# Optimization experiments

Hardware: AMD Instinct MI355X
Metric: run time of the kernel (lower is better)

The kernel has to match this reference:

```python
import jax, jax.numpy as jnp
import numpy as np

N_NODES = 50000
N_EDGES = 800000
N_GRAPHS = 256
D_IN, D_H1, D_H2, D_OUT = 64, 64, 64, 64


def gcn_conv(x, W, b, src, dst, n_nodes):
    # PyG GCNConv (eval): h = x @ W; add self-loops; deg[i] = in_deg(i) + 1;
    # out[i] = sum_{j->i} h[j] * deg[i]^-1/2 deg[j]^-1/2 + h[i]/deg[i] + b
    h = x @ W  # [N, F]
    ones = jnp.ones((src.shape[0],), dtype=x.dtype)
    deg = jax.ops.segment_sum(ones, dst, num_segments=n_nodes) + 1.0  # self loop
    dinv = jax.lax.rsqrt(deg)
    norm = dinv[src] * dinv[dst]  # [E]
    msg = h[src] * norm[:, None]  # [E, F]  (memory-bound gather)
    agg = jax.ops.segment_sum(msg, dst, num_segments=n_nodes)  # scatter-add
    agg = agg + h * (1.0 / deg)[:, None]  # self-loop contribution
    return agg + b


def setup_inputs() -> dict:
    key = jax.random.key(0)
    ks = jax.random.split(key, 12)
    x = jax.random.normal(ks[0], (N_NODES, D_IN), dtype=jnp.float32)
    src = jax.random.randint(ks[1], (N_EDGES,), 0, N_NODES)
    dst = jax.random.randint(ks[2], (N_EDGES,), 0, N_NODES)
    batch = jnp.sort(jax.random.randint(ks[3], (N_NODES,), 0, N_GRAPHS))
    def glorot(k, fin, fout):
        s = jnp.sqrt(6.0 / (fin + fout))
        return jax.random.uniform(k, (fin, fout), jnp.float32, -s, s)
    return {
        "x": x, "src": src, "dst": dst, "batch": batch,
        "W1": glorot(ks[4], D_IN, D_H1), "b1": jnp.zeros((D_H1,), jnp.float32),
        "W2": glorot(ks[5], D_H1, D_H2), "b2": jnp.zeros((D_H2,), jnp.float32),
        "W3": glorot(ks[6], D_H2, D_OUT), "b3": jnp.zeros((D_OUT,), jnp.float32),
        "Wl": glorot(ks[7], D_OUT, 1), "bl": jnp.zeros((1,), jnp.float32),
    }


def reference(x, src, dst, batch, W1, b1, W2, b2, W3, b3, Wl, bl):
    n = x.shape[0]
    h = jax.nn.relu(gcn_conv(x, W1, b1, src, dst, n))   # dropout inactive (eval)
    h = jax.nn.relu(gcn_conv(h, W2, b2, src, dst, n))
    h = jax.nn.relu(gcn_conv(h, W3, b3, src, dst, n))
    # global_mean_pool over graph ids
    sums = jax.ops.segment_sum(h, batch, num_segments=N_GRAPHS)  # [G, F]
    cnt = jax.ops.segment_sum(jnp.ones((n,), h.dtype), batch, num_segments=N_GRAPHS)
    pooled = sums / jnp.maximum(cnt, 1.0)[:, None]
    return pooled @ Wl + bl  # [G, 1]
```

## Files before the change

kernel.cpp:

```cpp
#include <hip/hip_runtime.h>

#define N_NODES 50000
#define N_EDGES 800000
#define N_GRAPHS 256
#define F 64
#define NBUCK 196
#define CAP 5120
#define P3_TILE 2048
#define P3_GRID ((N_EDGES + P3_TILE - 1) / P3_TILE)
#define BCAP 6144
#define ZOFF (N_NODES * 128)

__device__ __forceinline__ unsigned short f2bf(float f) {
    union { float f; unsigned u; } c; c.f = f;
    unsigned u = c.u + 0x7FFFu + ((c.u >> 16) & 1u);
    return (unsigned short)(u >> 16);
}
__device__ __forceinline__ unsigned pack2bf(float lo, float hi) {
    return (unsigned)f2bf(lo) | ((unsigned)f2bf(hi) << 16);
}
__device__ __forceinline__ float bfl(unsigned u) {
    union { unsigned u; float f; } c; c.u = u << 16; return c.f;
}
__device__ __forceinline__ float bfh(unsigned u) {
    union { unsigned u; float f; } c; c.u = u & 0xFFFF0000u; return c.f;
}

__device__ __forceinline__ void gather_run(const int* __restrict__ eidx,
                                           const char* __restrict__ Hb,
                                           int beg, int end, int fo, float* a) {
#pragma unroll
    for (int i = 0; i < 8; ++i) a[i] = 0.f;
    int kb = (beg < end) ? beg : 0;
    int4 oc = *(const int4*)(eidx + kb);
    int k1 = beg + 4;
    int k1c = (k1 < end) ? k1 : kb;
    int4 on = *(const int4*)(eidx + k1c);
    uint4 pc = *(const uint4*)(Hb + oc.x + fo);
    uint4 qc = *(const uint4*)(Hb + oc.y + fo);
    uint4 rc = *(const uint4*)(Hb + oc.z + fo);
    uint4 wc = *(const uint4*)(Hb + oc.w + fo);
    for (int k = beg; k < end; k += 4) {
        int k2 = k + 8;
        int k2c = (k2 < end) ? k2 : kb;
        int4 of = *(const int4*)(eidx + k2c);
        uint4 pn = *(const uint4*)(Hb + on.x + fo);
        uint4 qn = *(const uint4*)(Hb + on.y + fo);
        uint4 rn = *(const uint4*)(Hb + on.z + fo);
        uint4 wn = *(const uint4*)(Hb + on.w + fo);
        a[0] += (bfl(pc.x) + bfl(qc.x)) + (bfl(rc.x) + bfl(wc.x));
        a[1] += (bfh(pc.x) + bfh(qc.x)) + (bfh(rc.x) + bfh(wc.x));
        a[2] += (bfl(pc.y) + bfl(qc.y)) + (bfl(rc.y) + bfl(wc.y));
        a[3] += (bfh(pc.y) + bfh(qc.y)) + (bfh(rc.y) + bfh(wc.y));
        a[4] += (bfl(pc.z) + bfl(qc.z)) + (bfl(rc.z) + bfl(wc.z));
        a[5] += (bfh(pc.z) + bfh(qc.z)) + (bfh(rc.z) + bfh(wc.z));
        a[6] += (bfl(pc.w) + bfl(qc.w)) + (bfl(rc.w) + bfl(wc.w));
        a[7] += (bfh(pc.w) + bfh(qc.w)) + (bfh(rc.w) + bfh(wc.w));
        oc = on; on = of;
        pc = pn; qc = qn; rc = rn; wc = wn;
    }
}

__global__ __launch_bounds__(256) void partition_edges(const int* __restrict__ src,
                                                       const int* __restrict__ dst,
                                                       int* __restrict__ bcur,
                                                       unsigned int* __restrict__ bpair) {
    __shared__ int bh[NBUCK], bloc[NBUCK], bpos[NBUCK];
    int t = threadIdx.x;
    int lo = blockIdx.x * P3_TILE;
    int hi = min(lo + P3_TILE, N_EDGES);
    for (int i = t; i < NBUCK; i += 256) { bh[i] = 0; bpos[i] = 0; }
    __syncthreads();
    for (int e = lo + t; e < hi; e += 256) atomicAdd(&bh[dst[e] >> 8], 1);
    __syncthreads();
    for (int i = t; i < NBUCK; i += 256)
        bloc[i] = bh[i] ? atomicAdd(&bcur[i], bh[i]) : 0;
    __syncthreads();
    for (int e = lo + t; e < hi; e += 256) {
        int d = dst[e];
        int b = d >> 8;
        int r = atomicAdd(&bpos[b], 1);
        bpair[(size_t)b * CAP + bloc[b] + r] = ((unsigned)src[e] << 8) | (unsigned)(d & 255);
    }
}

__global__ __launch_bounds__(256) void bucket_sort(const unsigned int* __restrict__ bpair,
                                                   const int* __restrict__ bcur,
                                                   int* __restrict__ eidx,
                                                   int* __restrict__ rbeg,
                                                   int* __restrict__ rend,
                                                   float* __restrict__ dinv,
                                                   unsigned short* __restrict__ Abf,
                                                   unsigned short* __restrict__ Bbf) {
    __shared__ int cnt[256], s[256], pos[256];
    __shared__ int lout[BCAP];
    int b = blockIdx.x, t = threadIdx.x;
    int base = b * CAP;
    int sz = bcur[b];

    if (b == 0 && t < 8) {
        ((uint4*)Abf)[(size_t)N_NODES * 8 + t] = make_uint4(0u, 0u, 0u, 0u);
        ((uint4*)Bbf)[(size_t)N_NODES * 8 + t] = make_uint4(0u, 0u, 0u, 0u);
    }

    cnt[t] = 0;
    __syncthreads();
    for (int i = t; i < sz; i += 256) atomicAdd(&cnt[bpair[base + i] & 255], 1);
    __syncthreads();
    int v = cnt[t];
    int pv = (v + 3) & ~3;
    s[t] = pv;
    __syncthreads();
    for (int off = 1; off < 256; off <<= 1) {
        int u = (t >= off) ? s[t - off] : 0;
        __syncthreads();
        s[t] += u;
        __syncthreads();
    }
    int excl = s[t] - pv;
    pos[t] = excl;
    int node = b * 256 + t;
    if (node < N_NODES) {
        rbeg[node] = base + excl;
        rend[node] = base + excl + pv;
        dinv[node] = 1.0f / sqrtf((float)v + 1.0f);
    }
    int padtot = s[255];
    __syncthreads();

    for (int i = t; i < sz; i += 256) {
        unsigned p = bpair[base + i];
        int r = atomicAdd(&pos[p & 255], 1);
        lout[r] = (int)((p >> 8) << 7);
    }
    __syncthreads();
    for (int j = v; j < pv; j++) lout[excl + j] = ZOFF;
    __syncthreads();
    for (int i = t; i < padtot; i += 256) eidx[base + i] = lout[i];
}

#define XSTRIDE 17
__global__ __launch_bounds__(256) void gemm64_f32(const float* __restrict__ X,
                                                  const float* __restrict__ W,
                                                  const float* __restrict__ dinv,
                                                  unsigned short* __restrict__ Hn, int n) {
    __shared__ float4 sW[64 * 16];
    __shared__ float4 sX[128 * XSTRIDE];
    int tid = threadIdx.x;
    int base = blockIdx.x * 128;

    const float4* W4 = (const float4*)W;
    for (int i = tid; i < 64 * 16; i += 256) sW[i] = W4[i];
    {
        const float4* X4 = (const float4*)X;
        for (int i = tid; i < 128 * 16; i += 256) {
            int r = i >> 4, kg = i & 15;
            int node = base + r;
            sX[r * XSTRIDE + kg] = (node < n) ? X4[(size_t)node * 16 + kg]
                                              : make_float4(0.f, 0.f, 0.f, 0.f);
        }
    }
    __syncthreads();

    int fg = tid & 15;
    int ng = tid >> 4;
    float4 acc[8];
#pragma unroll
    for (int ii = 0; ii < 8; ii++) acc[ii] = make_float4(0.f, 0.f, 0.f, 0.f);

    for (int kg = 0; kg < 16; kg++) {
        float4 xv[8];
#pragma unroll
        for (int ii = 0; ii < 8; ii++) xv[ii] = sX[(ng + 16 * ii) * XSTRIDE + kg];
#pragma unroll
        for (int kk = 0; kk < 4; kk++) {
            float4 wv = sW[(4 * kg + kk) * 16 + fg];
#pragma unroll
            for (int ii = 0; ii < 8; ii++) {
                float xs = (kk == 0) ? xv[ii].x : (kk == 1) ? xv[ii].y
                         : (kk == 2) ? xv[ii].z : xv[ii].w;
                acc[ii].x += wv.x * xs;
                acc[ii].y += wv.y * xs;
                acc[ii].z += wv.z * xs;
                acc[ii].w += wv.w * xs;
            }
        }
    }

    ushort4* H4 = (ushort4*)Hn;
#pragma unroll
    for (int ii = 0; ii < 8; ii++) {
        int node = base + ng + 16 * ii;
        if (node < n) {
            float d = dinv[node];
            float4 o = acc[ii];
            ushort4 u;
            u.x = f2bf(o.x * d); u.y = f2bf(o.y * d);
            u.z = f2bf(o.z * d); u.w = f2bf(o.w * d);
            H4[(size_t)node * 16 + fg] = u;
        }
    }
}

__global__ __launch_bounds__(256) void gather_gemm(const int* __restrict__ rbeg,
                                                   const int* __restrict__ rend,
                                                   const int* __restrict__ eidx,
                                                   const float* __restrict__ dinv,
                                                   const unsigned short* __restrict__ Hin,
                                                   const float* __restrict__ bias,
                                                   const float* __restrict__ W,
                                                   unsigned short* __restrict__ Hout, int n) {
    __shared__ float4 sW[64 * 16];
    const float4* W4 = (const float4*)W;
    for (int i = threadIdx.x; i < 64 * 16; i += 256) sW[i] = W4[i];
    __syncthreads();

    int wv = (blockIdx.x * blockDim.x + threadIdx.x) >> 6;
    if (wv * 8 >= n) return;
    int lane = threadIdx.x & 63;
    int ns = lane >> 3, f = lane & 7;
    int node = wv * 8 + ns;
    int beg = rbeg[node];
    int end = rend[node];
    const char* Hb = (const char*)Hin;

    float di = dinv[node];
    uint4 hs = *(const uint4*)(Hb + (size_t)node * 128 + f * 16);
    float4 bb0 = ((const float4*)bias)[2 * f];
    float4 bb1 = ((const float4*)bias)[2 * f + 1];

    float a[8];
    gather_run(eidx, Hb, beg, end, f * 16, a);

    float v[8];
    v[0] = fmaxf(di * (a[0] + bfl(hs.x)) + bb0.x, 0.f);
    v[1] = fmaxf(di * (a[1] + bfh(hs.x)) + bb0.y, 0.f);
    v[2] = fmaxf(di * (a[2] + bfl(hs.y)) + bb0.z, 0.f);
    v[3] = fmaxf(di * (a[3] + bfh(hs.y)) + bb0.w, 0.f);
    v[4] = fmaxf(di * (a[4] + bfl(hs.z)) + bb1.x, 0.f);
    v[5] = fmaxf(di * (a[5] + bfh(hs.z)) + bb1.y, 0.f);
    v[6] = fmaxf(di * (a[6] + bfl(hs.w)) + bb1.z, 0.f);
    v[7] = fmaxf(di * (a[7] + bfh(hs.w)) + bb1.w, 0.f);

    float y0 = 0.f, y1 = 0.f, y2 = 0.f, y3 = 0.f;
    float y4 = 0.f, y5 = 0.f, y6 = 0.f, y7 = 0.f;
    int pb = (lane & 56) << 2;
#pragma unroll
    for (int c = 0; c < 8; ++c) {
        int ad = pb + 4 * c;
#pragma unroll
        for (int j = 0; j < 8; ++j) {
            float hk = __int_as_float(
                __builtin_amdgcn_ds_bpermute(ad, __float_as_int(v[j])));
            float4 w0 = sW[(8 * c + j) * 16 + 2 * f];
            float4 w1 = sW[(8 * c + j) * 16 + 2 * f + 1];
            y0 += hk * w0.x; y1 += hk * w0.y; y2 += hk * w0.z; y3 += hk * w0.w;
            y4 += hk * w1.x; y5 += hk * w1.y; y6 += hk * w1.z; y7 += hk * w1.w;
        }
    }

    uint4 u;
    u.x = pack2bf(y0 * di, y1 * di);
    u.y = pack2bf(y2 * di, y3 * di);
    u.z = pack2bf(y4 * di, y5 * di);
    u.w = pack2bf(y6 * di, y7 * di);
    ((uint4*)Hout)[(size_t)node * 8 + f] = u;
}

__global__ __launch_bounds__(256) void gather_pool(const int* __restrict__ rbeg,
                                                   const int* __restrict__ rend,
                                                   const int* __restrict__ eidx,
                                                   const float* __restrict__ dinv,
                                                   const unsigned short* __restrict__ Hn,
                                                   const float* __restrict__ b,
                                                   const float* __restrict__ Wl,
                                                   float* __restrict__ pdot, int n) {
    int wv = (blockIdx.x * blockDim.x + threadIdx.x) >> 6;
    int lane = threadIdx.x & 63;
    int ns = lane >> 3, f = lane & 7;
    int node = wv * 8 + ns;
    bool valid = node < n;
    int nodec = valid ? node : 0;
    int beg = valid ? rbeg[node] : 0;
    int end = valid ? rend[node] : 0;
    const char* Hb = (const char*)Hn;

    float di = dinv[nodec];
    uint4 hs = *(const uint4*)(Hb + (size_t)nodec * 128 + f * 16);
    float4 b0 = ((const float4*)b)[2 * f];
    float4 b1 = ((const float4*)b)[2 * f + 1];
    float4 w0 = ((const float4*)Wl)[2 * f];
    float4 w1 = ((const float4*)Wl)[2 * f + 1];

    float a[8];
    gather_run(eidx, Hb, beg, end, f * 16, a);

    float d = 0.f;
    d += fmaxf(di * (a[0] + bfl(hs.x)) + b0.x, 0.f) * w0.x;
    d += fmaxf(di * (a[1] + bfh(hs.x)) + b0.y, 0.f) * w0.y;
    d += fmaxf(di * (a[2] + bfl(hs.y)) + b0.z, 0.f) * w0.z;
    d += fmaxf(di * (a[3] + bfh(hs.y)) + b0.w, 0.f) * w0.w;
    d += fmaxf(di * (a[4] + bfl(hs.z)) + b1.x, 0.f) * w1.x;
    d += fmaxf(di * (a[5] + bfh(hs.z)) + b1.y, 0.f) * w1.y;
    d += fmaxf(di * (a[6] + bfl(hs.w)) + b1.z, 0.f) * w1.z;
    d += fmaxf(di * (a[7] + bfh(hs.w)) + b1.w, 0.f) * w1.w;
#pragma unroll
    for (int m = 1; m <= 4; m <<= 1) d += __shfl_xor(d, m);
    if (valid && f == 0) pdot[node] = d;
}

__global__ __launch_bounds__(64) void final_out(const float* __restrict__ pdot,
                                                const int* __restrict__ batch,
                                                const float* __restrict__ bl,
                                                float* __restrict__ out) {
    int g = blockIdx.x;
    __shared__ int slo, shi;
    int lane = threadIdx.x;
    if (lane == 0) {
        int a = 0, b = N_NODES;
        while (a < b) { int m = (a + b) >> 1; if (batch[m] < g) a = m + 1; else b = m; }
        slo = a;
        b = N_NODES;
        while (a < b) { int m = (a + b) >> 1; if (batch[m] < g + 1) a = m + 1; else b = m; }
        shi = a;
    }
    __syncthreads();
    int lo = slo, hi = shi;
    float acc = 0.f;
    for (int i = lo + lane; i < hi; i += 64) acc += pdot[i];
#pragma unroll
    for (int off = 32; off > 0; off >>= 1) acc += __shfl_down(acc, off);
    if (lane == 0) {
        float cnt = (float)(hi - lo);
        out[g] = acc / fmaxf(cnt, 1.0f) + bl[0];
    }
}

extern "C" void kernel_launch(void* const* d_in, const int* in_sizes, int n_in,
                              void* d_out, int out_size, void* d_ws, size_t ws_size,
                              hipStream_t stream) {
    const float* x     = (const float*)d_in[0];
    const int*   src   = (const int*)d_in[1];
    const int*   dst   = (const int*)d_in[2];
    const int*   batch = (const int*)d_in[3];
    const float* W1 = (const float*)d_in[4];  const float* b1 = (const float*)d_in[5];
    const float* W2 = (const float*)d_in[6];  const float* b2 = (const float*)d_in[7];
    const float* W3 = (const float*)d_in[8];  const float* b3 = (const float*)d_in[9];
    const float* Wl = (const float*)d_in[10]; const float* bl = (const float*)d_in[11];
    float* out = (float*)d_out;

    char* ws = (char*)d_ws;
    unsigned short* Abf = (unsigned short*)ws;
    unsigned short* Bbf = Abf + (size_t)(N_NODES + 1) * F;
    float* dinv    = (float*)(Bbf + (size_t)(N_NODES + 1) * F);
    float* pdot    = dinv + N_NODES;
    int*   rbeg    = (int*)(pdot + N_NODES);
    int*   rend    = rbeg + N_NODES;
    int*   bcur    = rend + N_NODES;
    unsigned int* bpair = (unsigned int*)(bcur + NBUCK);
    int*   eidx    = (int*)(bpair + (size_t)NBUCK * CAP);

    const int GEMM_GRID   = (N_NODES + 127) / 128;
    const int GATHER_GRID = (N_NODES + 31) / 32;

    hipMemsetAsync(bcur, 0, NBUCK * sizeof(int), stream);
    partition_edges<<<P3_GRID, 256, 0, stream>>>(src, dst, bcur, bpair);
    bucket_sort<<<NBUCK, 256, 0, stream>>>(bpair, bcur, eidx, rbeg, rend, dinv, Abf, Bbf);

    gemm64_f32<<<GEMM_GRID, 256, 0, stream>>>(x, W1, dinv, Abf, N_NODES);

    gather_gemm<<<GATHER_GRID, 256, 0, stream>>>(rbeg, rend, eidx, dinv, Abf, b1, W2, Bbf, N_NODES);

    gather_gemm<<<GATHER_GRID, 256, 0, stream>>>(rbeg, rend, eidx, dinv, Bbf, b2, W3, Abf, N_NODES);

    gather_pool<<<GATHER_GRID, 256, 0, stream>>>(rbeg, rend, eidx, dinv, Abf, b3, Wl, pdot, N_NODES);

    final_out<<<N_GRAPHS, 64, 0, stream>>>(pdot, batch, bl, out);
}
```

Before: 194.7 us.

## Split gather by source half across XCD groups and unfuse the dense GEMM

Edges for each destination are partitioned by whether their source node lies in the lower or upper half of the node range. The gather kernel sends lower-half work to XCDs 0-3 and upper-half work to XCDs 4-7, so each XCD's L2 only has to hold half of the bf16 feature table. Each half writes an fp32 partial aggregate to global memory. A separate templated GEMM kernel then combines the two partials with the self-loop, bias and ReLU before the next layer's matmul. This trades better gather cache locality for extra global traffic, since two full fp32 partial arrays are written and read back per layer. It also doubles edge padding and adds kernel launches.

```diff
diff --git a/kernel.cpp b/kernel.cpp
--- a/kernel.cpp
+++ b/kernel.cpp
@@ -5,11 +5,15 @@
 #define N_GRAPHS 256
 #define F 64
 #define NBUCK 196
-#define CAP 5120
+#define CAP 6656
 #define P3_TILE 2048
 #define P3_GRID ((N_EDGES + P3_TILE - 1) / P3_TILE)
-#define BCAP 6144
+#define BCAP 6656
 #define ZOFF (N_NODES * 128)
+#define NSPLIT 25000
+#define NSUB 1563
+#define GATHER_GRID (391 * 8)
+#define PDOT_GRID 1563
 
 __device__ __forceinline__ unsigned short f2bf(float f) {
     union { float f; unsigned u; } c; c.f = f;
@@ -87,29 +91,31 @@
 __global__ __launch_bounds__(256) void bucket_sort(const unsigned int* __restrict__ bpair,
                                                    const int* __restrict__ bcur,
                                                    int* __restrict__ eidx,
-                                                   int* __restrict__ rbeg,
-                                                   int* __restrict__ rend,
+                                                   int* __restrict__ rbegL,
+                                                   int* __restrict__ rendL,
+                                                   int* __restrict__ rbegH,
+                                                   int* __restrict__ rendH,
                                                    float* __restrict__ dinv,
-                                                   unsigned short* __restrict__ Abf,
-                                                   unsigned short* __restrict__ Bbf) {
-    __shared__ int cnt[256], s[256], pos[256];
+                                                   unsigned short* __restrict__ S) {
+    __shared__ int cntL[256], cntH[256], s[256], posL[256], posH[256];
     __shared__ int lout[BCAP];
     int b = blockIdx.x, t = threadIdx.x;
     int base = b * CAP;
     int sz = bcur[b];
 
-    if (b == 0 && t < 8) {
-        ((uint4*)Abf)[(size_t)N_NODES * 8 + t] = make_uint4(0u, 0u, 0u, 0u);
-        ((uint4*)Bbf)[(size_t)N_NODES * 8 + t] = make_uint4(0u, 0u, 0u, 0u);
-    }
-
-    cnt[t] = 0;
-    __syncthreads();
-    for (int i = t; i < sz; i += 256) atomicAdd(&cnt[bpair[base + i] & 255], 1);
-    __syncthreads();
-    int v = cnt[t];
-    int pv = (v + 3) & ~3;
-    s[t] = pv;
+    if (b == 0 && t < 8) ((uint4*)S)[(size_t)N_NODES * 8 + t] = make_uint4(0u, 0u, 0u, 0u);
+
+    cntL[t] = 0; cntH[t] = 0;
+    __syncthreads();
+    for (int i = t; i < sz; i += 256) {
+        unsigned p = bpair[base + i];
+        atomicAdd(((p >> 8) < (unsigned)NSPLIT) ? &cntL[p & 255] : &cntH[p & 255], 1);
+    }
+    __syncthreads();
+    int vL = cntL[t], vH = cntH[t];
+    int pvL = (vL + 3) & ~3;
+    int pvH = (vH + 3) & ~3;
+    s[t] = pvL + pvH;
     __syncthreads();
     for (int off = 1; off < 256; off <<= 1) {
         int u = (t >= off) ? s[t - off] : 0;
@@ -117,33 +123,43 @@
         s[t] += u;
         __syncthreads();
     }
-    int excl = s[t] - pv;
-    pos[t] = excl;
+    int excl = s[t] - (pvL + pvH);
+    posL[t] = excl;
+    posH[t] = excl + pvL;
     int node = b * 256 + t;
     if (node < N_NODES) {
-        rbeg[node] = base + excl;
-        rend[node] = base + excl + pv;
-        dinv[node] = 1.0f / sqrtf((float)v + 1.0f);
+        rbegL[node] = base + excl;
+        rendL[node] = base + excl + pvL;
+        rbegH[node] = base + excl + pvL;
+        rendH[node] = base + excl + pvL + pvH;
+        dinv[node] = 1.0f / sqrtf((float)(vL + vH) + 1.0f);
     }
     int padtot = s[255];
     __syncthreads();
 
     for (int i = t; i < sz; i += 256) {
         unsigned p = bpair[base + i];
-        int r = atomicAdd(&pos[p & 255], 1);
+        int d = p & 255;
+        int r = atomicAdd(((p >> 8) < (unsigned)NSPLIT) ? &posL[d] : &posH[d], 1);
         lout[r] = (int)((p >> 8) << 7);
     }
     __syncthreads();
-    for (int j = v; j < pv; j++) lout[excl + j] = ZOFF;
+    for (int j = vL; j < pvL; j++) lout[excl + j] = ZOFF;
+    for (int j = vH; j < pvH; j++) lout[excl + pvL + j] = ZOFF;
     __syncthreads();
     for (int i = t; i < padtot; i += 256) eidx[base + i] = lout[i];
 }
 
 #define XSTRIDE 17
-__global__ __launch_bounds__(256) void gemm64_f32(const float* __restrict__ X,
-                                                  const float* __restrict__ W,
-                                                  const float* __restrict__ dinv,
-                                                  unsigned short* __restrict__ Hn, int n) {
+template <int MODE>
+__global__ __launch_bounds__(256) void gemm64_t(const float* __restrict__ X,
+                                                const float* __restrict__ aggL,
+                                                const float* __restrict__ aggH,
+                                                const unsigned short* __restrict__ Sself,
+                                                const float* __restrict__ bias,
+                                                const float* __restrict__ W,
+                                                const float* __restrict__ dinv,
+                                                unsigned short* __restrict__ Sout, int n) {
     __shared__ float4 sW[64 * 16];
     __shared__ float4 sX[128 * XSTRIDE];
     int tid = threadIdx.x;
@@ -151,13 +167,34 @@
 
     const float4* W4 = (const float4*)W;
     for (int i = tid; i < 64 * 16; i += 256) sW[i] = W4[i];
-    {
+    if (MODE == 0) {
         const float4* X4 = (const float4*)X;
         for (int i = tid; i < 128 * 16; i += 256) {
             int r = i >> 4, kg = i & 15;
             int node = base + r;
             sX[r * XSTRIDE + kg] = (node < n) ? X4[(size_t)node * 16 + kg]
                                               : make_float4(0.f, 0.f, 0.f, 0.f);
+        }
+    } else {
+        const float4* L4 = (const float4*)aggL;
+        const float4* H4 = (const float4*)aggH;
+        const uint2* S2 = (const uint2*)Sself;
+        for (int i = tid; i < 128 * 16; i += 256) {
+            int r = i >> 4, kg = i & 15;
+            int node = base + r;
+            float4 hv = make_float4(0.f, 0.f, 0.f, 0.f);
+            if (node < n) {
+                float4 L = L4[(size_t)node * 16 + kg];
+                float4 Hh = H4[(size_t)node * 16 + kg];
+                uint2 su = S2[(size_t)node * 16 + kg];
+                float4 bb = ((const float4*)bias)[kg];
+                float di = dinv[node];
+                hv.x = fmaxf(di * (L.x + Hh.x + bfl(su.x)) + bb.x, 0.f);
+                hv.y = fmaxf(di * (L.y + Hh.y + bfh(su.x)) + bb.y, 0.f);
+                hv.z = fmaxf(di * (L.z + Hh.z + bfl(su.y)) + bb.z, 0.f);
+                hv.w = fmaxf(di * (L.w + Hh.w + bfh(su.y)) + bb.w, 0.f);
+            }
+            sX[r * XSTRIDE + kg] = hv;
         }
     }
     __syncthreads();
@@ -187,7 +224,7 @@
         }
     }
 
-    ushort4* H4 = (ushort4*)Hn;
+    ushort4* O4 = (ushort4*)Sout;
 #pragma unroll
     for (int ii = 0; ii < 8; ii++) {
         int node = base + ng + 16 * ii;
@@ -197,113 +234,80 @@
             ushort4 u;
             u.x = f2bf(o.x * d); u.y = f2bf(o.y * d);
             u.z = f2bf(o.z * d); u.w = f2bf(o.w * d);
-            H4[(size_t)node * 16 + fg] = u;
+            O4[(size_t)node * 16 + fg] = u;
         }
     }
 }
 
-__global__ __launch_bounds__(256) void gather_gemm(const int* __restrict__ rbeg,
-                                                   const int* __restrict__ rend,
-                                                   const int* __restrict__ eidx,
-                                                   const float* __restrict__ dinv,
-                                                   const unsigned short* __restrict__ Hin,
-                                                   const float* __restrict__ bias,
-                                                   const float* __restrict__ W,
-                                                   unsigned short* __restrict__ Hout, int n) {
-    __shared__ float4 sW[64 * 16];
-    const float4* W4 = (const float4*)W;
-    for (int i = threadIdx.x; i < 64 * 16; i += 256) sW[i] = W4[i];
-    __syncthreads();
-
-    int wv = (blockIdx.x * blockDim.x + threadIdx.x) >> 6;
-    if (wv * 8 >= n) return;
+__global__ __launch_bounds__(256) void gather_split(const int* __restrict__ rbegL,
+                                                    const int* __restrict__ rendL,
+                                                    const int* __restrict__ rbegH,
+                                                    const int* __restrict__ rendH,
+                                                    const int* __restrict__ eidx,
+                                                    const unsigned short* __restrict__ S,
+                                                    float* __restrict__ aggL,
+                                                    float* __restrict__ aggH) {
+    int bid = blockIdx.x;
+    int xcd = bid & 7;
+    int h = xcd >> 2;
+    int sub = (bid >> 3) * 4 + (xcd & 3);
+    if (sub >= NSUB) return;
+    int wid = threadIdx.x >> 6;
     int lane = threadIdx.x & 63;
     int ns = lane >> 3, f = lane & 7;
-    int node = wv * 8 + ns;
-    int beg = rbeg[node];
-    int end = rend[node];
-    const char* Hb = (const char*)Hin;
-
-    float di = dinv[node];
-    uint4 hs = *(const uint4*)(Hb + (size_t)node * 128 + f * 16);
-    float4 bb0 = ((const float4*)bias)[2 * f];
-    float4 bb1 = ((const float4*)bias)[2 * f + 1];
+    int node = sub * 32 + wid * 8 + ns;
+    bool valid = node < N_NODES;
+    int nodec = valid ? node : 0;
+    const int* rb = h ? rbegH : rbegL;
+    const int* re = h ? rendH : rendL;
+    int beg = valid ? rb[nodec] : 0;
+    int end = valid ? re[nodec] : 0;
 
     float a[8];
-    gather_run(eidx, Hb, beg, end, f * 16, a);
-
-    float v[8];
-    v[0] = fmaxf(di * (a[0] + bfl(hs.x)) + bb0.x, 0.f);
-    v[1] = fmaxf(di * (a[1] + bfh(hs.x)) + bb0.y, 0.f);
-    v[2] = fmaxf(di * (a[2] + bfl(hs.y)) + bb0.z, 0.f);
-    v[3] = fmaxf(di * (a[3] + bfh(hs.y)) + bb0.w, 0.f);
-    v[4] = fmaxf(di * (a[4] + bfl(hs.z)) + bb1.x, 0.f);
-    v[5] = fmaxf(di * (a[5] + bfh(hs.z)) + bb1.y, 0.f);
-    v[6] = fmaxf(di * (a[6] + bfl(hs.w)) + bb1.z, 0.f);
-    v[7] = fmaxf(di * (a[7] + bfh(hs.w)) + bb1.w, 0.f);
-
-    float y0 = 0.f, y1 = 0.f, y2 = 0.f, y3 = 0.f;
-    float y4 = 0.f, y5 = 0.f, y6 = 0.f, y7 = 0.f;
-    int pb = (lane & 56) << 2;
-#pragma unroll
-    for (int c = 0; c < 8; ++c) {
-        int ad = pb + 4 * c;
-#pragma unroll
-        for (int j = 0; j < 8; ++j) {
-            float hk = __int_as_float(
-                __builtin_amdgcn_ds_bpermute(ad, __float_as_int(v[j])));
-            float4 w0 = sW[(8 * c + j) * 16 + 2 * f];
-            float4 w1 = sW[(8 * c + j) * 16 + 2 * f + 1];
-            y0 += hk * w0.x; y1 += hk * w0.y; y2 += hk * w0.z; y3 += hk * w0.w;
-            y4 += hk * w1.x; y5 += hk * w1.y; y6 += hk * w1.z; y7 += hk * w1.w;
-        }
-    }
-
-    uint4 u;
-    u.x = pack2bf(y0 * di, y1 * di);
-    u.y = pack2bf(y2 * di, y3 * di);
-    u.z = pack2bf(y4 * di, y5 * di);
-    u.w = pack2bf(y6 * di, y7 * di);
-    ((uint4*)Hout)[(size_t)node * 8 + f] = u;
-}
-
-__global__ __launch_bounds__(256) void gather_pool(const int* __restrict__ rbeg,
-                                                   const int* __restrict__ rend,
-                                                   const int* __restrict__ eidx,
+    gather_run(eidx, (const char*)S, beg, end, f * 16, a);
+
+    if (valid) {
+        float* agg = h ? aggH : aggL;
+        float4* o = (float4*)(agg + (size_t)node * 64 + f * 8);
+        o[0] = make_float4(a[0], a[1], a[2], a[3]);
+        o[1] = make_float4(a[4], a[5], a[6], a[7]);
+    }
+}
+
+__global__ __launch_bounds__(256) void pdot_kernel(const float* __restrict__ aggL,
+                                                   const float* __restrict__ aggH,
+                                                   const unsigned short* __restrict__ S,
                                                    const float* __restrict__ dinv,
-                                                   const unsigned short* __restrict__ Hn,
-                                                   const float* __restrict__ b,
+                                                   const float* __restrict__ b3,
                                                    const float* __restrict__ Wl,
-                                                   float* __restrict__ pdot, int n) {
+                                                   float* __restrict__ pdot) {
     int wv = (blockIdx.x * blockDim.x + threadIdx.x) >> 6;
     int lane = threadIdx.x & 63;
     int ns = lane >> 3, f = lane & 7;
     int node = wv * 8 + ns;
-    bool valid = node < n;
+    bool valid = node < N_NODES;
     int nodec = valid ? node : 0;
-    int beg = valid ? rbeg[node] : 0;
-    int end = valid ? rend[node] : 0;
-    const char* Hb = (const char*)Hn;
 
     float di = dinv[nodec];
-    uint4 hs = *(const uint4*)(Hb + (size_t)nodec * 128 + f * 16);
-    float4 b0 = ((const float4*)b)[2 * f];
-    float4 b1 = ((const float4*)b)[2 * f + 1];
+    const float4* L4 = (const float4*)(aggL + (size_t)nodec * 64 + f * 8);
+    const float4* H4 = (const float4*)(aggH + (size_t)nodec * 64 + f * 8);
+    float4 L0 = L4[0], L1 = L4[1];
+    float4 H0 = H4[0], H1 = H4[1];
+    uint4 su = *(const uint4*)((const char*)S + (size_t)nodec * 128 + f * 16);
+    float4 bb0 = ((const float4*)b3)[2 * f];
+    float4 bb1 = ((const float4*)b3)[2 * f + 1];
     float4 w0 = ((const float4*)Wl)[2 * f];
     float4 w1 = ((const float4*)Wl)[2 * f + 1];
 
-    float a[8];
-    gather_run(eidx, Hb, beg, end, f * 16, a);
-
     float d = 0.f;
-    d += fmaxf(di * (a[0] + bfl(hs.x)) + b0.x, 0.f) * w0.x;
-    d += fmaxf(di * (a[1] + bfh(hs.x)) + b0.y, 0.f) * w0.y;
-    d += fmaxf(di * (a[2] + bfl(hs.y)) + b0.z, 0.f) * w0.z;
-    d += fmaxf(di * (a[3] + bfh(hs.y)) + b0.w, 0.f) * w0.w;
-    d += fmaxf(di * (a[4] + bfl(hs.z)) + b1.x, 0.f) * w1.x;
-    d += fmaxf(di * (a[5] + bfh(hs.z)) + b1.y, 0.f) * w1.y;
-    d += fmaxf(di * (a[6] + bfl(hs.w)) + b1.z, 0.f) * w1.z;
-    d += fmaxf(di * (a[7] + bfh(hs.w)) + b1.w, 0.f) * w1.w;
+    d += fmaxf(di * (L0.x + H0.x + bfl(su.x)) + bb0.x, 0.f) * w0.x;
+    d += fmaxf(di * (L0.y + H0.y + bfh(su.x)) + bb0.y, 0.f) * w0.y;
+    d += fmaxf(di * (L0.z + H0.z + bfl(su.y)) + bb0.z, 0.f) * w0.z;
+    d += fmaxf(di * (L0.w + H0.w + bfh(su.y)) + bb0.w, 0.f) * w0.w;
+    d += fmaxf(di * (L1.x + H1.x + bfl(su.z)) + bb1.x, 0.f) * w1.x;
+    d += fmaxf(di * (L1.y + H1.y + bfh(su.z)) + bb1.y, 0.f) * w1.y;
+    d += fmaxf(di * (L1.z + H1.z + bfl(su.w)) + bb1.z, 0.f) * w1.z;
+    d += fmaxf(di * (L1.w + H1.w + bfh(su.w)) + bb1.w, 0.f) * w1.w;
 #pragma unroll
     for (int m = 1; m <= 4; m <<= 1) d += __shfl_xor(d, m);
     if (valid && f == 0) pdot[node] = d;
@@ -350,30 +354,34 @@
     float* out = (float*)d_out;
 
     char* ws = (char*)d_ws;
-    unsigned short* Abf = (unsigned short*)ws;
-    unsigned short* Bbf = Abf + (size_t)(N_NODES + 1) * F;
-    float* dinv    = (float*)(Bbf + (size_t)(N_NODES + 1) * F);
-    float* pdot    = dinv + N_NODES;
-    int*   rbeg    = (int*)(pdot + N_NODES);
-    int*   rend    = rbeg + N_NODES;
-    int*   bcur    = rend + N_NODES;
+    unsigned short* S = (unsigned short*)ws;
+    float* aggL   = (float*)(S + (size_t)(N_NODES + 1) * F);
+    float* aggH   = aggL + (size_t)N_NODES * F;
+    float* dinv   = aggH + (size_t)N_NODES * F;
+    float* pdot   = dinv + N_NODES;
+    int*   rbegL  = (int*)(pdot + N_NODES);
+    int*   rendL  = rbegL + N_NODES;
+    int*   rbegH  = rendL + N_NODES;
+    int*   rendH  = rbegH + N_NODES;
+    int*   bcur   = rendH + N_NODES;
     unsigned int* bpair = (unsigned int*)(bcur + NBUCK);
-    int*   eidx    = (int*)(bpair + (size_t)NBUCK * CAP);
-
-    const int GEMM_GRID   = (N_NODES + 127) / 128;
-    const int GATHER_GRID = (N_NODES + 31) / 32;
+    int*   eidx   = (int*)(bpair + (size_t)NBUCK * CAP);
+
+    const int GEMM_GRID = (N_NODES + 127) / 128;
 
     hipMemsetAsync(bcur, 0, NBUCK * sizeof(int), stream);
     partition_edges<<<P3_GRID, 256, 0, stream>>>(src, dst, bcur, bpair);
-    bucket_sort<<<NBUCK, 256, 0, stream>>>(bpair, bcur, eidx, rbeg, rend, dinv, Abf, Bbf);
-
-    gemm64_f32<<<GEMM_GRID, 256, 0, stream>>>(x, W1, dinv, Abf, N_NODES);
-
-    gather_gemm<<<GATHER_GRID, 256, 0, stream>>>(rbeg, rend, eidx, dinv, Abf, b1, W2, Bbf, N_NODES);
-
-    gather_gemm<<<GATHER_GRID, 256, 0, stream>>>(rbeg, rend, eidx, dinv, Bbf, b2, W3, Abf, N_NODES);
-
-    gather_pool<<<GATHER_GRID, 256, 0, stream>>>(rbeg, rend, eidx, dinv, Abf, b3, Wl, pdot, N_NODES);
-
+    bucket_sort<<<NBUCK, 256, 0, stream>>>(bpair, bcur, eidx, rbegL, rendL, rbegH, rendH, dinv, S);
+
+    gemm64_t<0><<<GEMM_GRID, 256, 0, stream>>>(x, nullptr, nullptr, nullptr, nullptr, W1, dinv, S, N_NODES);
+    gather_split<<<GATHER_GRID, 256, 0, stream>>>(rbegL, rendL, rbegH, rendH, eidx, S, aggL, aggH);
+
+    gemm64_t<1><<<GEMM_GRID, 256, 0, stream>>>(nullptr, aggL, aggH, S, b1, W2, dinv, S, N_NODES);
+    gather_split<<<GATHER_GRID, 256, 0, stream>>>(rbegL, rendL, rbegH, rendH, eidx, S, aggL, aggH);
+
+    gemm64_t<1><<<GEMM_GRID, 256, 0, stream>>>(nullptr, aggL, aggH, S, b2, W3, dinv, S, N_NODES);
+    gather_split<<<GATHER_GRID, 256, 0, stream>>>(rbegL, rendL, rbegH, rendH, eidx, S, aggL, aggH);
+
+    pdot_kernel<<<PDOT_GRID, 256, 0, stream>>>(aggL, aggH, S, dinv, b3, Wl, pdot);
     final_out<<<N_GRAPHS, 64, 0, stream>>>(pdot, batch, bl, out);
 }
```

Result: slower. 211.2 us (+8.5%).
